# Optimization experiments

Hardware: AMD Instinct MI355X
Metric: run time of the kernel (lower is better)

Reference implementation:

```python
import jax, jax.numpy as jnp
import numpy as np

N = 1_000_000          # total nodes (atoms)
F = 32                 # node feature dim
K = 16                 # kernels per degree
DEG_COUNTS = [200_000, 300_000, 300_000, 200_000]  # focal nodes per degree 1..4
EPS = 1e-8


def _unit(a):
    # L2-normalize along last axis (CosineSimilarity semantics)
    return a / (jnp.linalg.norm(a, axis=-1, keepdims=True) + EPS)


def setup_inputs() -> dict:
    key = jax.random.key(0)
    ks = jax.random.split(key, 16)
    x = jax.random.normal(ks[0], (N, F), dtype=jnp.float32)
    # selected indices: disjoint partition of all nodes by degree (a permutation)
    perm = jax.random.permutation(ks[1], N)
    sels, off = [], 0
    for c in DEG_COUNTS:
        sels.append(perm[off:off + c].astype(jnp.int64))
        off += c
    inp = {"x": x}
    for d in range(1, 5):
        inp[f"selected_index_deg{d}"] = sels[d - 1]
        inp[f"nei_index_deg{d}"] = jax.random.randint(
            ks[1 + d], (d * DEG_COUNTS[d - 1],), 0, N).astype(jnp.int64)
        inp[f"W_focal{d}"] = jax.random.normal(ks[7 + d], (K, F), dtype=jnp.float32)
        inp[f"W_nei{d}"] = jax.random.normal(ks[11 + d], (K, d, F), dtype=jnp.float32)
    return inp


def _degree_score(x, sel, nei, Wf, Wn, deg):
    # gather receptive field for this degree group
    x_focal = _unit(x[sel])                         # (Nd, F)
    x_nei = _unit(x[nei].reshape(-1, deg, F))       # (Nd, deg, F)
    sc_f = _unit(Wf) @ x_focal.T                    # (K, Nd) cosine vs focal kernel
    sc_n = jnp.einsum('kdf,ndf->kn', _unit(Wn), x_nei) / deg  # mean neighbor cosine
    return sc_f + sc_n                              # (K, Nd)


def reference(x,
              W_focal1, W_nei1, W_focal2, W_nei2,
              W_focal3, W_nei3, W_focal4, W_nei4,
              selected_index_deg1, selected_index_deg2,
              selected_index_deg3, selected_index_deg4,
              nei_index_deg1, nei_index_deg2,
              nei_index_deg3, nei_index_deg4):
    sels = [selected_index_deg1, selected_index_deg2,
            selected_index_deg3, selected_index_deg4]
    neis = [nei_index_deg1, nei_index_deg2, nei_index_deg3, nei_index_deg4]
    Wfs = [W_focal1, W_focal2, W_focal3, W_focal4]
    Wns = [W_nei1, W_nei2, W_nei3, W_nei4]

    out = jnp.zeros((4 * K, N), dtype=x.dtype)  # the `zeros` score matrix
    row, col = 0, 0
    for d in range(1, 5):
        sc = _degree_score(x, sels[d - 1], neis[d - 1], Wfs[d - 1], Wns[d - 1], d)
        nd = sels[d - 1].shape[0]
        out = out.at[row:row + K, col:col + nd].set(sc)
        row += K
        col += nd
    # reorder columns back to original node order (get_reorder_index -> sort)
    order = jnp.argsort(jnp.concatenate(sels))
    return out[:, order].T  # (N, 4*K)
```

## Files before the change

kernel.cpp:

```cpp
#include <hip/hip_runtime.h>
#include <math.h>

#define F 32
#define K 16
#define EPSN 1e-8f

__device__ __forceinline__ float dot4(const float4 a, const float4 b) {
    return a.x*b.x + a.y*b.y + a.z*b.z + a.w*b.w;
}

template<int DEG>
__device__ __forceinline__ void process_deg(const float* __restrict__ x,
                                            const int*   __restrict__ sel,
                                            const int*   __restrict__ nei,
                                            const float* __restrict__ Wf,
                                            const float* __restrict__ Wn,
                                            float* __restrict__ out,
                                            int nd, int i0, float* sW)
{
    constexpr int NW = K * (1 + DEG);
    const int tid = threadIdx.x;

    if (tid < NW) {
        const float* src = (tid < K) ? (Wf + tid * F) : (Wn + (tid - K) * F);
        float ss = 0.f;
        #pragma unroll
        for (int f = 0; f < F; ++f) { float v = src[f]; ss += v * v; }
        const float sc = 1.f / (sqrtf(ss) + EPSN);
        #pragma unroll
        for (int f = 0; f < F; ++f) sW[tid * F + f] = src[f] * sc;
    }
    __syncthreads();

    const int quad  = tid >> 2;
    const int p     = tid & 3;
    const int pbase = p * 8;

    #pragma unroll 1
    for (int it = 0; it < 4; ++it) {
        const int i = i0 + it * 64 + quad;
        if (i >= nd) continue;

        const int node = sel[i];
        int nn[DEG];
        #pragma unroll
        for (int j = 0; j < DEG; ++j) nn[j] = nei[i * DEG + j];

        float acc[K];

        #pragma unroll
        for (int r = 0; r <= DEG; ++r) {
            const unsigned row = (unsigned)((r == 0) ? node : nn[r - 1]);
            const float* xr = x + row * (unsigned)F + pbase;
            const float4 rv0 = *(const float4*)(xr);
            const float4 rv1 = *(const float4*)(xr + 4);

            float ss = dot4(rv0, rv0) + dot4(rv1, rv1);
            ss += __shfl_xor(ss, 1);
            ss += __shfl_xor(ss, 2);
            float sc = 1.f / (sqrtf(ss) + EPSN);
            if (r > 0) sc *= (1.f / (float)DEG);

            #pragma unroll
            for (int k = 0; k < K; ++k) {
                const int wrow = (r == 0) ? k : (K + k * DEG + (r - 1));
                const float4 w0 = *(const float4*)&sW[wrow * F + pbase];
                const float4 w1 = *(const float4*)&sW[wrow * F + pbase + 4];
                const float d = dot4(w0, rv0) + dot4(w1, rv1);
                if (r == 0) acc[k] = d * sc;
                else        acc[k] = fmaf(d, sc, acc[k]);
            }
        }

        #pragma unroll
        for (int k = 0; k < K; ++k) {
            acc[k] += __shfl_xor(acc[k], 1);
            acc[k] += __shfl_xor(acc[k], 2);
        }

        float4* o = (float4*)(out + (size_t)node * (4 * K) + p * 16);
        if (p == DEG - 1) {
            o[0] = make_float4(acc[0],  acc[1],  acc[2],  acc[3]);
            o[1] = make_float4(acc[4],  acc[5],  acc[6],  acc[7]);
            o[2] = make_float4(acc[8],  acc[9],  acc[10], acc[11]);
            o[3] = make_float4(acc[12], acc[13], acc[14], acc[15]);
        } else {
            const float4 z = make_float4(0.f, 0.f, 0.f, 0.f);
            o[0] = z; o[1] = z; o[2] = z; o[3] = z;
        }
    }
}

struct Args {
    const float* x;
    const int*   sel[4];
    const int*   nei[4];
    const float* Wf[4];
    const float* Wn[4];
    int nd[4];
    int bcum[4];
};

__global__ __launch_bounds__(256)
void fused_kernel(Args a, float* __restrict__ out)
{
    __shared__ float sW[K * 5 * F];
    const int bid = blockIdx.x;

    if (bid < a.bcum[0]) {
        process_deg<1>(a.x, a.sel[0], a.nei[0], a.Wf[0], a.Wn[0], out,
                       a.nd[0], bid * 256, sW);
    } else if (bid < a.bcum[1]) {
        process_deg<2>(a.x, a.sel[1], a.nei[1], a.Wf[1], a.Wn[1], out,
                       a.nd[1], (bid - a.bcum[0]) * 256, sW);
    } else if (bid < a.bcum[2]) {
        process_deg<3>(a.x, a.sel[2], a.nei[2], a.Wf[2], a.Wn[2], out,
                       a.nd[2], (bid - a.bcum[1]) * 256, sW);
    } else {
        process_deg<4>(a.x, a.sel[3], a.nei[3], a.Wf[3], a.Wn[3], out,
                       a.nd[3], (bid - a.bcum[2]) * 256, sW);
    }
}

extern "C" void kernel_launch(void* const* d_in, const int* in_sizes, int n_in,
                              void* d_out, int out_size, void* d_ws, size_t ws_size,
                              hipStream_t stream)
{
    Args a;
    a.x = (const float*)d_in[0];
    for (int d = 0; d < 4; ++d) {
        a.sel[d] = (const int*)  d_in[1 + 4 * d];
        a.nei[d] = (const int*)  d_in[2 + 4 * d];
        a.Wf[d]  = (const float*)d_in[3 + 4 * d];
        a.Wn[d]  = (const float*)d_in[4 + 4 * d];
        a.nd[d]  = in_sizes[1 + 4 * d];
    }
    int cum = 0;
    for (int d = 0; d < 4; ++d) {
        cum += (a.nd[d] + 255) / 256;
        a.bcum[d] = cum;
    }
    float* out = (float*)d_out;
    fused_kernel<<<cum, 256, 0, stream>>>(a, out);
}
```

Measured before the change: 491.5 us.

## Compute kernel-cosine scores with MFMA f16 split-precision matrix ops

```diff
diff --git a/kernel.cpp b/kernel.cpp
--- a/kernel.cpp
+++ b/kernel.cpp
@@ -5,9 +5,9 @@
 #define K 16
 #define EPSN 1e-8f
 
-__device__ __forceinline__ float dot4(const float4 a, const float4 b) {
-    return a.x*b.x + a.y*b.y + a.z*b.z + a.w*b.w;
-}
+
+typedef _Float16 half8 __attribute__((ext_vector_type(8)));
+typedef float f32x4  __attribute__((ext_vector_type(4)));
 
 template<int DEG>
 __device__ __forceinline__ void process_deg(const float* __restrict__ x,
@@ -16,77 +16,97 @@
                                             const float* __restrict__ Wf,
                                             const float* __restrict__ Wn,
                                             float* __restrict__ out,
-                                            int nd, int i0, float* sW)
+                                            int nd, int i0,
+                                            _Float16* sWh, _Float16* sWl)
 {
-    constexpr int NW = K * (1 + DEG);
+    constexpr int R  = 1 + DEG;
+    constexpr int NW = K * R;
     const int tid = threadIdx.x;
 
     if (tid < NW) {
         const float* src = (tid < K) ? (Wf + tid * F) : (Wn + (tid - K) * F);
         float ss = 0.f;
         #pragma unroll
-        for (int f = 0; f < F; ++f) { float v = src[f]; ss += v * v; }
+        for (int f = 0; f < F; ++f) { const float t = src[f]; ss += t * t; }
         const float sc = 1.f / (sqrtf(ss) + EPSN);
+        const int t = tid - K;
+        const int r = (tid < K) ? 0   : (1 + t % DEG);
+        const int k = (tid < K) ? tid : (t / DEG);
         #pragma unroll
-        for (int f = 0; f < F; ++f) sW[tid * F + f] = src[f] * sc;
+        for (int f = 0; f < F; ++f) {
+            const float wv = src[f] * sc;
+            const _Float16 hi = (_Float16)wv;
+            const _Float16 lo = (_Float16)(wv - (float)hi);
+            const int off = r * 512 + (k + 16 * (f >> 3)) * 8 + (f & 7);
+            sWh[off] = hi; sWl[off] = lo;
+        }
     }
     __syncthreads();
 
-    const int quad  = tid >> 2;
-    const int p     = tid & 3;
-    const int pbase = p * 8;
+    const int lane = tid & 63;
+    const int wv   = tid >> 6;
+    const int jcol = lane & 15;
+    const int kq   = lane >> 4;
+    const float invdeg = 1.f / (float)DEG;
 
     #pragma unroll 1
     for (int it = 0; it < 4; ++it) {
-        const int i = i0 + it * 64 + quad;
-        if (i >= nd) continue;
+        int i = i0 + it * 64 + wv * 16 + jcol;
+        const bool valid = (i < nd);
+        if (!valid) i = nd - 1;
 
         const int node = sel[i];
         int nn[DEG];
         #pragma unroll
         for (int j = 0; j < DEG; ++j) nn[j] = nei[i * DEG + j];
 
-        float acc[K];
+        f32x4 acc = {0.f, 0.f, 0.f, 0.f};
 
         #pragma unroll
-        for (int r = 0; r <= DEG; ++r) {
+        for (int r = 0; r < R; ++r) {
             const unsigned row = (unsigned)((r == 0) ? node : nn[r - 1]);
-            const float* xr = x + row * (unsigned)F + pbase;
-            const float4 rv0 = *(const float4*)(xr);
-            const float4 rv1 = *(const float4*)(xr + 4);
+            const float* xr = x + row * (unsigned)F + kq * 8;
+            const float4 a0 = *(const float4*)(xr);
+            const float4 a1 = *(const float4*)(xr + 4);
 
-            float ss = dot4(rv0, rv0) + dot4(rv1, rv1);
-            ss += __shfl_xor(ss, 1);
-            ss += __shfl_xor(ss, 2);
+            float ss = a0.x*a0.x + a0.y*a0.y + a0.z*a0.z + a0.w*a0.w
+                     + a1.x*a1.x + a1.y*a1.y + a1.z*a1.z + a1.w*a1.w;
+            ss += __shfl_xor(ss, 16);
+            ss += __shfl_xor(ss, 32);
             float sc = 1.f / (sqrtf(ss) + EPSN);
-            if (r > 0) sc *= (1.f / (float)DEG);
+            if (r > 0) sc *= invdeg;
 
-            #pragma unroll
-            for (int k = 0; k < K; ++k) {
-                const int wrow = (r == 0) ? k : (K + k * DEG + (r - 1));
-                const float4 w0 = *(const float4*)&sW[wrow * F + pbase];
-                const float4 w1 = *(const float4*)&sW[wrow * F + pbase + 4];
-                const float d = dot4(w0, rv0) + dot4(w1, rv1);
-                if (r == 0) acc[k] = d * sc;
-                else        acc[k] = fmaf(d, sc, acc[k]);
-            }
+            const float f0 = a0.x*sc, f1 = a0.y*sc, f2 = a0.z*sc, f3 = a0.w*sc;
+            const float f4 = a1.x*sc, f5 = a1.y*sc, f6 = a1.z*sc, f7 = a1.w*sc;
+
+            half8 bh, bl;
+            bh[0]=(_Float16)f0; bl[0]=(_Float16)(f0-(float)bh[0]);
+            bh[1]=(_Float16)f1; bl[1]=(_Float16)(f1-(float)bh[1]);
+            bh[2]=(_Float16)f2; bl[2]=(_Float16)(f2-(float)bh[2]);
+            bh[3]=(_Float16)f3; bl[3]=(_Float16)(f3-(float)bh[3]);
+            bh[4]=(_Float16)f4; bl[4]=(_Float16)(f4-(float)bh[4]);
+            bh[5]=(_Float16)f5; bl[5]=(_Float16)(f5-(float)bh[5]);
+            bh[6]=(_Float16)f6; bl[6]=(_Float16)(f6-(float)bh[6]);
+            bh[7]=(_Float16)f7; bl[7]=(_Float16)(f7-(float)bh[7]);
+
+            const int aoff = r * 512 + lane * 8;
+            const half8 ah = *(const half8*)(sWh + aoff);
+            const half8 al = *(const half8*)(sWl + aoff);
+
+            acc = __builtin_amdgcn_mfma_f32_16x16x32_f16(ah, bh, acc, 0, 0, 0);
+            acc = __builtin_amdgcn_mfma_f32_16x16x32_f16(ah, bl, acc, 0, 0, 0);
+            acc = __builtin_amdgcn_mfma_f32_16x16x32_f16(al, bh, acc, 0, 0, 0);
         }
 
-        #pragma unroll
-        for (int k = 0; k < K; ++k) {
-            acc[k] += __shfl_xor(acc[k], 1);
-            acc[k] += __shfl_xor(acc[k], 2);
-        }
-
-        float4* o = (float4*)(out + (size_t)node * (4 * K) + p * 16);
-        if (p == DEG - 1) {
-            o[0] = make_float4(acc[0],  acc[1],  acc[2],  acc[3]);
-            o[1] = make_float4(acc[4],  acc[5],  acc[6],  acc[7]);
-            o[2] = make_float4(acc[8],  acc[9],  acc[10], acc[11]);
-            o[3] = make_float4(acc[12], acc[13], acc[14], acc[15]);
-        } else {
-            const float4 z = make_float4(0.f, 0.f, 0.f, 0.f);
-            o[0] = z; o[1] = z; o[2] = z; o[3] = z;
+        if (valid) {
+            float* orow = out + (size_t)node * (4 * K);
+            #pragma unroll
+            for (int b = 0; b < 4; ++b) {
+                float4 vst = make_float4(0.f, 0.f, 0.f, 0.f);
+                if (b == DEG - 1)
+                    vst = make_float4(acc[0], acc[1], acc[2], acc[3]);
+                *(float4*)(orow + (b * 4 + kq) * 4) = vst;
+            }
         }
     }
 }
@@ -104,21 +124,22 @@
 __global__ __launch_bounds__(256)
 void fused_kernel(Args a, float* __restrict__ out)
 {
-    __shared__ float sW[K * 5 * F];
+    __shared__ __align__(16) _Float16 sWh[5 * 512];
+    __shared__ __align__(16) _Float16 sWl[5 * 512];
     const int bid = blockIdx.x;
 
     if (bid < a.bcum[0]) {
         process_deg<1>(a.x, a.sel[0], a.nei[0], a.Wf[0], a.Wn[0], out,
-                       a.nd[0], bid * 256, sW);
+                       a.nd[0], bid * 256, sWh, sWl);
     } else if (bid < a.bcum[1]) {
         process_deg<2>(a.x, a.sel[1], a.nei[1], a.Wf[1], a.Wn[1], out,
-                       a.nd[1], (bid - a.bcum[0]) * 256, sW);
+                       a.nd[1], (bid - a.bcum[0]) * 256, sWh, sWl);
     } else if (bid < a.bcum[2]) {
         process_deg<3>(a.x, a.sel[2], a.nei[2], a.Wf[2], a.Wn[2], out,
-                       a.nd[2], (bid - a.bcum[1]) * 256, sW);
+                       a.nd[2], (bid - a.bcum[1]) * 256, sWh, sWl);
     } else {
         process_deg<4>(a.x, a.sel[3], a.nei[3], a.Wf[3], a.Wn[3], out,
-                       a.nd[3], (bid - a.bcum[2]) * 256, sW);
+                       a.nd[3], (bid - a.bcum[2]) * 256, sWh, sWl);
     }
 }
 
```

Result: faster. 443.0 us (-9.9%).
